# Optimization experiments

Measured on AMD Instinct MI355X. Metric: run time of the kernel, lower is better.

## Reference

```python
import jax, jax.numpy as jnp
import numpy as np

N = 50000      # nodes
E = 800000     # edges
INS = 128
H = 128
OUTS = 128
G = 512        # graphs in batch
BN_EPS = 1e-5


def _lin(k, fan_in, fan_out):
    s = 1.0 / np.sqrt(fan_in)
    kw, kb = jax.random.split(k)
    w = jax.random.uniform(kw, (fan_in, fan_out), minval=-s, maxval=s, dtype=jnp.float32)
    b = jax.random.uniform(kb, (fan_out,), minval=-s, maxval=s, dtype=jnp.float32)
    return w, b


def setup_inputs() -> dict:
    key = jax.random.key(0)
    ks = jax.random.split(key, 16)
    x = jax.random.normal(ks[0], (N, INS), dtype=jnp.float32)
    edge_src = jax.random.randint(ks[1], (E,), 0, N, dtype=jnp.int32)
    edge_dst = jax.random.randint(ks[2], (E,), 0, N, dtype=jnp.int32)
    ptr = jnp.sort(jax.random.randint(ks[3], (G + 1,), 0, N, dtype=jnp.int32))
    ptr = ptr.at[0].set(0).at[-1].set(N)
    w1a, b1a = _lin(ks[4], INS, H)
    w1b, b1b = _lin(ks[5], H, H)
    w2a, b2a = _lin(ks[6], H, H)
    w2b, b2b = _lin(ks[7], H, H)
    w3a, b3a = _lin(ks[8], H, H)
    w3b, b3b = _lin(ks[9], H, OUTS)
    g1 = jnp.ones((H,), jnp.float32); be1 = jnp.zeros((H,), jnp.float32)
    g2 = jnp.ones((H,), jnp.float32); be2 = jnp.zeros((H,), jnp.float32)
    g3 = jnp.ones((H,), jnp.float32); be3 = jnp.zeros((H,), jnp.float32)
    return dict(x=x, edge_src=edge_src, edge_dst=edge_dst, ptr=ptr,
                w1a=w1a, b1a=b1a, g1=g1, be1=be1, w1b=w1b, b1b=b1b,
                w2a=w2a, b2a=b2a, g2=g2, be2=be2, w2b=w2b, b2b=b2b,
                w3a=w3a, b3a=b3a, g3=g3, be3=be3, w3b=w3b, b3b=b3b)


def _bn(h, gamma, beta):
    # BatchNorm1d in training mode: stats over the node dimension
    mu = jnp.mean(h, axis=0)
    var = jnp.var(h, axis=0)
    return gamma * (h - mu) * jax.lax.rsqrt(var + BN_EPS) + beta


def _gin_layer(h, src, dst, wa, ba, gamma, beta, wb, bb):
    # GINConv (eps=0): mlp(x + sum_{j in N(i)} x_j)
    agg = jax.ops.segment_sum(h[src], dst, num_segments=N)  # [N, d]
    h = h + agg
    h = jax.nn.relu(_bn(h @ wa + ba, gamma, beta))
    h = jax.nn.relu(h @ wb + bb)
    return h


def reference(x, edge_src, edge_dst, ptr,
              w1a, b1a, g1, be1, w1b, b1b,
              w2a, b2a, g2, be2, w2b, b2b,
              w3a, b3a, g3, be3, w3b, b3b):
    h = _gin_layer(x, edge_src, edge_dst, w1a, b1a, g1, be1, w1b, b1b)
    h = _gin_layer(h, edge_src, edge_dst, w2a, b2a, g2, be2, w2b, b2b)
    h = _gin_layer(h, edge_src, edge_dst, w3a, b3a, g3, be3, w3b, b3b)
    # segment_csr(x, ptr, reduce='sum') readout
    seg = jnp.searchsorted(ptr, jnp.arange(N, dtype=jnp.int32), side='right') - 1
    return jax.ops.segment_sum(h, seg, num_segments=G)  # [G, OUTS]
```

## Files before the change

### kernel.cpp

```cpp
#include <hip/hip_runtime.h>

#define NNODES 50000
#define NEDGES 800000
#define HD 128
#define NG 512
#define BN_EPS 1e-5f
#define NTILE 3125
#define NSPLIT 8
#define NSB 49
#define AROW 136

typedef short bf16x8 __attribute__((ext_vector_type(8)));
typedef float floatx4 __attribute__((ext_vector_type(4)));

union U16 { uint4 u; bf16x8 h; };

__device__ __forceinline__ ushort f2bf(float f) {
    unsigned u = __float_as_uint(f);
    return (ushort)((u + 0x7fffu + ((u >> 16) & 1u)) >> 16);
}
__device__ __forceinline__ void unpack8(const uint4& u, float* f) {
    const unsigned* w = (const unsigned*)&u;
#pragma unroll
    for (int i = 0; i < 4; ++i) {
        f[2 * i]     = __uint_as_float(w[i] << 16);
        f[2 * i + 1] = __uint_as_float(w[i] & 0xffff0000u);
    }
}
__device__ __forceinline__ uint4 pack8(const float* f) {
    uint4 o;
    unsigned* w = (unsigned*)&o;
#pragma unroll
    for (int i = 0; i < 4; ++i)
        w[i] = (unsigned)f2bf(f[2 * i]) | ((unsigned)f2bf(f[2 * i + 1]) << 16);
    return o;
}


struct WP6 { const float* w[6]; };

__global__ __launch_bounds__(256) void prep_kernel(
    const int* __restrict__ edst, int* __restrict__ cnt,
    const float* __restrict__ x, ushort* __restrict__ xb,
    WP6 p, ushort* __restrict__ wf) {
    const int b = blockIdx.x, t = threadIdx.x;
    if (b < 3125) {
        atomicAdd(&cnt[edst[b * 256 + t]], 1);
    } else if (b < 9375) {
        int i = (b - 3125) * 256 + t;
        float4 v = ((const float4*)x)[i];
        ushort4 o;
        o.x = f2bf(v.x); o.y = f2bf(v.y); o.z = f2bf(v.z); o.w = f2bf(v.w);
        ((ushort4*)xb)[i] = o;
    } else {
        int m = b - 9375;
        const float* W = p.w[m];
        ushort* o = wf + (size_t)m * 16384;
        for (int i = t; i < 16384; i += 256) {
            int j = i & 7, lane = (i >> 3) & 63, kc = (i >> 9) & 3, ct = i >> 11;
            int k = kc * 32 + (lane >> 4) * 8 + j;
            int n = ct * 16 + (lane & 15);
            o[i] = f2bf(W[k * HD + n]);
        }
    }
}


__global__ void scan1_kernel(const int* __restrict__ cnt, int* __restrict__ incl,
                             int* __restrict__ bsum, int n) {
    __shared__ int s[1024];
    int i = blockIdx.x * 1024 + threadIdx.x;
    int v = (i < n) ? cnt[i] : 0;
    s[threadIdx.x] = v;
    __syncthreads();
    for (int off = 1; off < 1024; off <<= 1) {
        int add = (threadIdx.x >= off) ? s[threadIdx.x - off] : 0;
        __syncthreads();
        s[threadIdx.x] += add;
        __syncthreads();
    }
    if (i < n) incl[i] = s[threadIdx.x];
    if (threadIdx.x == 1023) bsum[blockIdx.x] = s[1023];
}

__global__ void scan23_kernel(const int* __restrict__ incl, const int* __restrict__ bsum,
                              int* __restrict__ rowp, int n) {
    __shared__ int bpre[64];
    const int t = threadIdx.x;
    if (t < 64) {
        int own = (t < NSB) ? bsum[t] : 0;
        int v = own;
        for (int off = 1; off < 64; off <<= 1) {
            int u = __shfl_up(v, off);
            if (t >= off) v += u;
        }
        bpre[t] = v - own;
    }
    __syncthreads();
    int i = blockIdx.x * 256 + t;
    if (i < n) rowp[i + 1] = incl[i] + bpre[i >> 10];
    if (i == 0) rowp[0] = 0;
}

__global__ void build_kernel(const int* __restrict__ src, const int* __restrict__ dst,
                             const int* __restrict__ rowp, int* __restrict__ fill,
                             int* __restrict__ colv, int n) {
    int i = blockIdx.x * 256 + threadIdx.x;
    if (i < n) {
        int d = dst[i];
        int pos = rowp[d] + atomicAdd(&fill[d], 1);
        colv[pos] = src[i];
    }
}


__global__ __launch_bounds__(256, 4) void gemmA_kernel(
    const ushort* __restrict__ H, const int* __restrict__ rowp,
    const int* __restrict__ colv, const ushort* __restrict__ Wf,
    const float* __restrict__ bias, ushort* __restrict__ out,
    float* __restrict__ ssum_p, float* __restrict__ ssq_p) {
    __shared__ ushort abuf[16 * AROW];
    __shared__ ushort cbuf[16 * HD];
    __shared__ float reds[HD];
    __shared__ float redq[HD];
    const int t = threadIdx.x;
    const int wave = t >> 6, lane = t & 63;
    const int quad = lane >> 4, l16 = lane & 15;
    const int row0 = blockIdx.x * 16;

    const uint4* Wf4 = (const uint4*)Wf;
    uint4 bfr[2][4];
#pragma unroll
    for (int c = 0; c < 2; ++c)
#pragma unroll
        for (int kc = 0; kc < 4; ++kc)
            bfr[c][kc] = Wf4[((2 * wave + c) * 4 + kc) * 64 + lane];

    {
        int nl = t >> 4;
        int node = row0 + nl;
        int l = t & 15;
        int beg = rowp[node], end = rowp[node + 1];
        const uint4* hp = (const uint4*)H;
        float a[8];
        unpack8(hp[(size_t)node * 16 + l], a);
        for (int j = beg; j < end; ++j) {
            float b[8];
            unpack8(hp[(size_t)colv[j] * 16 + l], b);
#pragma unroll
            for (int i = 0; i < 8; ++i) a[i] += b[i];
        }
        *(uint4*)&abuf[nl * AROW + l * 8] = pack8(a);
    }
    __syncthreads();

    U16 afr[4];
#pragma unroll
    for (int kc = 0; kc < 4; ++kc)
        afr[kc].u = *(const uint4*)&abuf[l16 * AROW + kc * 32 + quad * 8];

    floatx4 zf = {0.f, 0.f, 0.f, 0.f};
    floatx4 acc[2] = {zf, zf};
#pragma unroll
    for (int kc = 0; kc < 4; ++kc) {
#pragma unroll
        for (int c = 0; c < 2; ++c) {
            U16 bu;
            bu.u = bfr[c][kc];
            acc[c] = __builtin_amdgcn_mfma_f32_16x16x32_bf16(afr[kc].h, bu.h, acc[c], 0, 0, 0);
        }
    }

    const int lrow = quad * 4;
#pragma unroll
    for (int c = 0; c < 2; ++c) {
        int col = (2 * wave + c) * 16 + l16;
        float b = bias[col];
        float s = 0.f, q = 0.f;
#pragma unroll
        for (int reg = 0; reg < 4; ++reg) {
            float v = acc[c][reg] + b;
            cbuf[(lrow + reg) * HD + col] = f2bf(v);
            s += v; q += v * v;
        }
        s += __shfl_xor(s, 16); s += __shfl_xor(s, 32);
        q += __shfl_xor(q, 16); q += __shfl_xor(q, 32);
        if (quad == 0) { reds[col] = s; redq[col] = q; }
    }
    __syncthreads();

    {
        const uint4* c4 = (const uint4*)cbuf;
        uint4* o4 = (uint4*)out;
        int row = t >> 4, part = t & 15;
        o4[(size_t)(row0 + row) * 16 + part] = c4[t];
    }

    int slot = (blockIdx.x & (NSPLIT - 1)) * HD;
    if (t < HD) atomicAdd(&ssum_p[slot + t], reds[t]);
    else        atomicAdd(&ssq_p[slot + (t - HD)], redq[t - HD]);
}


template <bool READOUT>
__global__ __launch_bounds__(256, 4) void gemmB_kernel(
    const ushort* __restrict__ A, const ushort* __restrict__ Wf,
    const float* __restrict__ bias, ushort* __restrict__ out,
    const float* __restrict__ gamma, const float* __restrict__ beta,
    const float* __restrict__ ssum_p, const float* __restrict__ ssq_p,
    const int* __restrict__ gptr, float* __restrict__ gout) {
    __shared__ ushort cbuf[16 * HD];
    __shared__ float sca[HD];
    __shared__ float shf[HD];
    const int t = threadIdx.x;
    const int wave = t >> 6, lane = t & 63;
    const int quad = lane >> 4, l16 = lane & 15;
    const int row0 = blockIdx.x * 16;
    const int rowA = row0 + l16;

    const uint4* Wf4 = (const uint4*)Wf;
    uint4 bfr[2][4];
#pragma unroll
    for (int c = 0; c < 2; ++c)
#pragma unroll
        for (int kc = 0; kc < 4; ++kc)
            bfr[c][kc] = Wf4[((2 * wave + c) * 4 + kc) * 64 + lane];

    U16 afr[4];
    {
        const ushort* ap = A + (size_t)rowA * HD + quad * 8;
#pragma unroll
        for (int kc = 0; kc < 4; ++kc)
            afr[kc].u = *(const uint4*)(ap + kc * 32);
    }

    if (t < HD) {
        float s = 0.f, q = 0.f;
#pragma unroll
        for (int i = 0; i < NSPLIT; ++i) { s += ssum_p[i * HD + t]; q += ssq_p[i * HD + t]; }
        float mean = s / (float)NNODES;
        float var = q / (float)NNODES - mean * mean;
        float rstd = rsqrtf(var + BN_EPS);
        float sc = gamma[t] * rstd;
        sca[t] = sc;
        shf[t] = beta[t] - mean * sc;
    }
    __syncthreads();

#pragma unroll
    for (int kc = 0; kc < 4; ++kc) {
        float f[8];
        unpack8(afr[kc].u, f);
        int kb = kc * 32 + quad * 8;
        float4 s0 = ((const float4*)(sca + kb))[0];
        float4 s1 = ((const float4*)(sca + kb))[1];
        float4 h0 = ((const float4*)(shf + kb))[0];
        float4 h1 = ((const float4*)(shf + kb))[1];
        f[0] = fmaxf(fmaf(f[0], s0.x, h0.x), 0.f);
        f[1] = fmaxf(fmaf(f[1], s0.y, h0.y), 0.f);
        f[2] = fmaxf(fmaf(f[2], s0.z, h0.z), 0.f);
        f[3] = fmaxf(fmaf(f[3], s0.w, h0.w), 0.f);
        f[4] = fmaxf(fmaf(f[4], s1.x, h1.x), 0.f);
        f[5] = fmaxf(fmaf(f[5], s1.y, h1.y), 0.f);
        f[6] = fmaxf(fmaf(f[6], s1.z, h1.z), 0.f);
        f[7] = fmaxf(fmaf(f[7], s1.w, h1.w), 0.f);
        afr[kc].u = pack8(f);
    }

    floatx4 zf = {0.f, 0.f, 0.f, 0.f};
    floatx4 acc[2] = {zf, zf};
#pragma unroll
    for (int kc = 0; kc < 4; ++kc) {
#pragma unroll
        for (int c = 0; c < 2; ++c) {
            U16 bu;
            bu.u = bfr[c][kc];
            acc[c] = __builtin_amdgcn_mfma_f32_16x16x32_bf16(afr[kc].h, bu.h, acc[c], 0, 0, 0);
        }
    }

    if (READOUT) {
        int r_base = row0 + quad * 4;
        int lo = 0, hi = NG - 1;
        while (lo < hi) {
            int mid = (lo + hi) >> 1;
            if (r_base >= gptr[mid + 1]) lo = mid + 1; else hi = mid;
        }
        int segr[4];
        int sg = lo;
#pragma unroll
        for (int reg = 0; reg < 4; ++reg) {
            while (r_base + reg >= gptr[sg + 1]) ++sg;
            segr[reg] = sg;
        }
#pragma unroll
        for (int c = 0; c < 2; ++c) {
            int col = (2 * wave + c) * 16 + l16;
            float b = bias[col];
            float run = 0.f;
            int cur = segr[0];
#pragma unroll
            for (int reg = 0; reg < 4; ++reg) {
                if (segr[reg] != cur) {
                    if (run != 0.f) atomicAdd(&gout[cur * HD + col], run);
                    run = 0.f;
                    cur = segr[reg];
                }
                run += fmaxf(acc[c][reg] + b, 0.f);
            }
            if (run != 0.f) atomicAdd(&gout[cur * HD + col], run);
        }
        return;
    }

    const int lrow = quad * 4;
#pragma unroll
    for (int c = 0; c < 2; ++c) {
        int col = (2 * wave + c) * 16 + l16;
        float b = bias[col];
#pragma unroll
        for (int reg = 0; reg < 4; ++reg)
            cbuf[(lrow + reg) * HD + col] = f2bf(fmaxf(acc[c][reg] + b, 0.f));
    }
    __syncthreads();
    {
        const uint4* c4 = (const uint4*)cbuf;
        uint4* o4 = (uint4*)out;
        int row = t >> 4, part = t & 15;
        o4[(size_t)(row0 + row) * 16 + part] = c4[t];
    }
}


extern "C" void kernel_launch(void* const* d_in, const int* in_sizes, int n_in,
                              void* d_out, int out_size, void* d_ws, size_t ws_size,
                              hipStream_t stream) {
    const float* x = (const float*)d_in[0];
    const int* esrc = (const int*)d_in[1];
    const int* edst = (const int*)d_in[2];
    const int* gptr = (const int*)d_in[3];
    const float* wA[3] = {(const float*)d_in[4], (const float*)d_in[10], (const float*)d_in[16]};
    const float* bA[3] = {(const float*)d_in[5], (const float*)d_in[11], (const float*)d_in[17]};
    const float* gm[3] = {(const float*)d_in[6], (const float*)d_in[12], (const float*)d_in[18]};
    const float* bt[3] = {(const float*)d_in[7], (const float*)d_in[13], (const float*)d_in[19]};
    const float* wB[3] = {(const float*)d_in[8], (const float*)d_in[14], (const float*)d_in[20]};
    const float* bB[3] = {(const float*)d_in[9], (const float*)d_in[15], (const float*)d_in[21]};

    char* w = (char*)d_ws;
    ushort* xb   = (ushort*)w; w += (size_t)NNODES * HD * 2;
    ushort* zbb  = (ushort*)w; w += (size_t)NNODES * HD * 2;
    ushort* hbb  = (ushort*)w; w += (size_t)NNODES * HD * 2;
    ushort* wf   = (ushort*)w; w += (size_t)6 * 16384 * 2;
    int* colv  = (int*)w;   w += (size_t)NEDGES * 4;
    int* incl  = (int*)w;   w += (size_t)NNODES * 4;
    int* rowp  = (int*)w;   w += ((size_t)(NNODES + 1) * 4 + 15) & ~(size_t)15;
    int* bsum  = (int*)w;   w += 64 * 4;
    char* zero_base = w;
    int* cnt   = (int*)w;   w += (size_t)NNODES * 4;
    int* fill  = (int*)w;   w += (size_t)NNODES * 4;
    float* ssum_p = (float*)w; w += 3 * NSPLIT * 128 * 4;
    float* ssq_p  = (float*)w; w += 3 * NSPLIT * 128 * 4;
    size_t zero_bytes = (size_t)(w - zero_base);

    hipMemsetAsync(zero_base, 0, zero_bytes, stream);
    hipMemsetAsync(d_out, 0, (size_t)NG * HD * 4, stream);

    WP6 wp;
    wp.w[0] = wA[0]; wp.w[1] = wB[0]; wp.w[2] = wA[1];
    wp.w[3] = wB[1]; wp.w[4] = wA[2]; wp.w[5] = wB[2];

    prep_kernel<<<9381, 256, 0, stream>>>(edst, cnt, x, xb, wp, wf);
    scan1_kernel<<<NSB, 1024, 0, stream>>>(cnt, incl, bsum, NNODES);
    scan23_kernel<<<(NNODES + 255) / 256, 256, 0, stream>>>(incl, bsum, rowp, NNODES);
    build_kernel<<<(NEDGES + 255) / 256, 256, 0, stream>>>(esrc, edst, rowp, fill, colv, NEDGES);

    const ushort* hin = xb;
    for (int l = 0; l < 3; ++l) {
        gemmA_kernel<<<NTILE, 256, 0, stream>>>(
            hin, rowp, colv, wf + (size_t)(2 * l) * 16384, bA[l], zbb,
            ssum_p + l * NSPLIT * 128, ssq_p + l * NSPLIT * 128);
        if (l < 2) {
            gemmB_kernel<false><<<NTILE, 256, 0, stream>>>(
                zbb, wf + (size_t)(2 * l + 1) * 16384, bB[l], hbb, gm[l], bt[l],
                ssum_p + l * NSPLIT * 128, ssq_p + l * NSPLIT * 128, nullptr, nullptr);
        } else {
            gemmB_kernel<true><<<NTILE, 256, 0, stream>>>(
                zbb, wf + (size_t)(2 * l + 1) * 16384, bB[l], nullptr, gm[l], bt[l],
                ssum_p + l * NSPLIT * 128, ssq_p + l * NSPLIT * 128, gptr, (float*)d_out);
        }
        hin = hbb;
    }
}
```

Baseline: 422.0 us.

## Apply first linear before aggregation and fuse next layer's A-GEMM into B-GEMM

Uses linearity, (h+A h)W = hW + A(hW), so each layer's first GEMM runs before the neighbour gather. The gather kernel then sums projected rows, adds the bias and accumulates BN statistics, and each B-GEMM is fused with the following layer's A-GEMM, with that weight staged in LDS. The fp32-to-bf16 conversion of x moves into the first GEMM, and the CSR build reuses per-edge ranks from the counting atomics instead of a second atomic pass. The cost is an extra rank array, more LDS per block (lower occupancy), and rounding the projected features to bf16 before aggregation.

```diff
diff --git a/kernel.cpp b/kernel.cpp
--- a/kernel.cpp
+++ b/kernel.cpp
@@ -40,20 +40,14 @@
 struct WP6 { const float* w[6]; };
 
 __global__ __launch_bounds__(256) void prep_kernel(
-    const int* __restrict__ edst, int* __restrict__ cnt,
-    const float* __restrict__ x, ushort* __restrict__ xb,
+    const int* __restrict__ edst, int* __restrict__ cnt, int* __restrict__ rank,
     WP6 p, ushort* __restrict__ wf) {
     const int b = blockIdx.x, t = threadIdx.x;
     if (b < 3125) {
-        atomicAdd(&cnt[edst[b * 256 + t]], 1);
-    } else if (b < 9375) {
-        int i = (b - 3125) * 256 + t;
-        float4 v = ((const float4*)x)[i];
-        ushort4 o;
-        o.x = f2bf(v.x); o.y = f2bf(v.y); o.z = f2bf(v.z); o.w = f2bf(v.w);
-        ((ushort4*)xb)[i] = o;
+        int i = b * 256 + t;
+        rank[i] = atomicAdd(&cnt[edst[i]], 1);
     } else {
-        int m = b - 9375;
+        int m = b - 3125;
         const float* W = p.w[m];
         ushort* o = wf + (size_t)m * 16384;
         for (int i = t; i < 16384; i += 256) {
@@ -103,26 +97,18 @@
 }
 
 __global__ void build_kernel(const int* __restrict__ src, const int* __restrict__ dst,
-                             const int* __restrict__ rowp, int* __restrict__ fill,
+                             const int* __restrict__ rowp, const int* __restrict__ rank,
                              int* __restrict__ colv, int n) {
     int i = blockIdx.x * 256 + threadIdx.x;
-    if (i < n) {
-        int d = dst[i];
-        int pos = rowp[d] + atomicAdd(&fill[d], 1);
-        colv[pos] = src[i];
-    }
-}
-
-
-__global__ __launch_bounds__(256, 4) void gemmA_kernel(
-    const ushort* __restrict__ H, const int* __restrict__ rowp,
-    const int* __restrict__ colv, const ushort* __restrict__ Wf,
-    const float* __restrict__ bias, ushort* __restrict__ out,
-    float* __restrict__ ssum_p, float* __restrict__ ssq_p) {
+    if (i < n) colv[rowp[dst[i]] + rank[i]] = src[i];
+}
+
+
+__global__ __launch_bounds__(256, 4) void gemm0A_kernel(
+    const float* __restrict__ x, const ushort* __restrict__ Wf,
+    ushort* __restrict__ y) {
     __shared__ ushort abuf[16 * AROW];
     __shared__ ushort cbuf[16 * HD];
-    __shared__ float reds[HD];
-    __shared__ float redq[HD];
     const int t = threadIdx.x;
     const int wave = t >> 6, lane = t & 63;
     const int quad = lane >> 4, l16 = lane & 15;
@@ -137,20 +123,12 @@
             bfr[c][kc] = Wf4[((2 * wave + c) * 4 + kc) * 64 + lane];
 
     {
-        int nl = t >> 4;
-        int node = row0 + nl;
-        int l = t & 15;
-        int beg = rowp[node], end = rowp[node + 1];
-        const uint4* hp = (const uint4*)H;
-        float a[8];
-        unpack8(hp[(size_t)node * 16 + l], a);
-        for (int j = beg; j < end; ++j) {
-            float b[8];
-            unpack8(hp[(size_t)colv[j] * 16 + l], b);
-#pragma unroll
-            for (int i = 0; i < 8; ++i) a[i] += b[i];
-        }
-        *(uint4*)&abuf[nl * AROW + l * 8] = pack8(a);
+        int r = t >> 4, l = t & 15;
+        const float* xp = x + (size_t)(row0 + r) * HD + l * 8;
+        float4 v0 = ((const float4*)xp)[0];
+        float4 v1 = ((const float4*)xp)[1];
+        float f[8] = {v0.x, v0.y, v0.z, v0.w, v1.x, v1.y, v1.z, v1.w};
+        *(uint4*)&abuf[r * AROW + l * 8] = pack8(f);
     }
     __syncthreads();
 
@@ -162,54 +140,94 @@
     floatx4 zf = {0.f, 0.f, 0.f, 0.f};
     floatx4 acc[2] = {zf, zf};
 #pragma unroll
-    for (int kc = 0; kc < 4; ++kc) {
+    for (int kc = 0; kc < 4; ++kc)
 #pragma unroll
         for (int c = 0; c < 2; ++c) {
-            U16 bu;
-            bu.u = bfr[c][kc];
+            U16 bu; bu.u = bfr[c][kc];
             acc[c] = __builtin_amdgcn_mfma_f32_16x16x32_bf16(afr[kc].h, bu.h, acc[c], 0, 0, 0);
         }
-    }
 
     const int lrow = quad * 4;
 #pragma unroll
     for (int c = 0; c < 2; ++c) {
         int col = (2 * wave + c) * 16 + l16;
-        float b = bias[col];
-        float s = 0.f, q = 0.f;
-#pragma unroll
-        for (int reg = 0; reg < 4; ++reg) {
-            float v = acc[c][reg] + b;
-            cbuf[(lrow + reg) * HD + col] = f2bf(v);
-            s += v; q += v * v;
-        }
-        s += __shfl_xor(s, 16); s += __shfl_xor(s, 32);
-        q += __shfl_xor(q, 16); q += __shfl_xor(q, 32);
-        if (quad == 0) { reds[col] = s; redq[col] = q; }
-    }
-    __syncthreads();
-
+#pragma unroll
+        for (int reg = 0; reg < 4; ++reg)
+            cbuf[(lrow + reg) * HD + col] = f2bf(acc[c][reg]);
+    }
+    __syncthreads();
     {
         const uint4* c4 = (const uint4*)cbuf;
-        uint4* o4 = (uint4*)out;
+        uint4* o4 = (uint4*)y;
         int row = t >> 4, part = t & 15;
         o4[(size_t)(row0 + row) * 16 + part] = c4[t];
     }
-
+}
+
+
+__global__ __launch_bounds__(256) void agg_kernel(
+    const ushort* __restrict__ y, const int* __restrict__ rowp,
+    const int* __restrict__ colv, const float* __restrict__ bias,
+    ushort* __restrict__ z, float* __restrict__ ssum_p, float* __restrict__ ssq_p) {
+    __shared__ float reds[4][HD];
+    __shared__ float redq[4][HD];
+    const int t = threadIdx.x;
+    const int wave = t >> 6, lane = t & 63;
+    const int node = blockIdx.x * 16 + (t >> 4);
+    const int l = t & 15;
+    const uint4* hp = (const uint4*)y;
+
+    float a[8];
+    unpack8(hp[(size_t)node * 16 + l], a);
+    int beg = rowp[node], end = rowp[node + 1];
+    for (int j = beg; j < end; ++j) {
+        float b[8];
+        unpack8(hp[(size_t)colv[j] * 16 + l], b);
+#pragma unroll
+        for (int i = 0; i < 8; ++i) a[i] += b[i];
+    }
+    {
+        float4 b0 = ((const float4*)(bias + l * 8))[0];
+        float4 b1 = ((const float4*)(bias + l * 8))[1];
+        a[0] += b0.x; a[1] += b0.y; a[2] += b0.z; a[3] += b0.w;
+        a[4] += b1.x; a[5] += b1.y; a[6] += b1.z; a[7] += b1.w;
+    }
+    ((uint4*)z)[(size_t)node * 16 + l] = pack8(a);
+
+    float s[8], q[8];
+#pragma unroll
+    for (int i = 0; i < 8; ++i) { s[i] = a[i]; q[i] = a[i] * a[i]; }
+#pragma unroll
+    for (int i = 0; i < 8; ++i) {
+        s[i] += __shfl_xor(s[i], 16); s[i] += __shfl_xor(s[i], 32);
+        q[i] += __shfl_xor(q[i], 16); q[i] += __shfl_xor(q[i], 32);
+    }
+    if (lane < 16) {
+#pragma unroll
+        for (int i = 0; i < 8; ++i) {
+            reds[wave][lane * 8 + i] = s[i];
+            redq[wave][lane * 8 + i] = q[i];
+        }
+    }
+    __syncthreads();
     int slot = (blockIdx.x & (NSPLIT - 1)) * HD;
-    if (t < HD) atomicAdd(&ssum_p[slot + t], reds[t]);
-    else        atomicAdd(&ssq_p[slot + (t - HD)], redq[t - HD]);
-}
-
-
-template <bool READOUT>
-__global__ __launch_bounds__(256, 4) void gemmB_kernel(
-    const ushort* __restrict__ A, const ushort* __restrict__ Wf,
-    const float* __restrict__ bias, ushort* __restrict__ out,
+    if (t < HD) {
+        atomicAdd(&ssum_p[slot + t], reds[0][t] + reds[1][t] + reds[2][t] + reds[3][t]);
+    } else if (t < 2 * HD) {
+        int c = t - HD;
+        atomicAdd(&ssq_p[slot + c], redq[0][c] + redq[1][c] + redq[2][c] + redq[3][c]);
+    }
+}
+
+
+__global__ __launch_bounds__(256, 3) void gemmBA_kernel(
+    const ushort* __restrict__ z, const ushort* __restrict__ WfB,
+    const ushort* __restrict__ WfA2, const float* __restrict__ biasB,
+    ushort* __restrict__ yout,
     const float* __restrict__ gamma, const float* __restrict__ beta,
-    const float* __restrict__ ssum_p, const float* __restrict__ ssq_p,
-    const int* __restrict__ gptr, float* __restrict__ gout) {
-    __shared__ ushort cbuf[16 * HD];
+    const float* __restrict__ ssum_p, const float* __restrict__ ssq_p) {
+    __shared__ ushort was[16384];
+    __shared__ ushort cbuf[16 * AROW];
     __shared__ float sca[HD];
     __shared__ float shf[HD];
     const int t = threadIdx.x;
@@ -218,7 +236,17 @@
     const int row0 = blockIdx.x * 16;
     const int rowA = row0 + l16;
 
-    const uint4* Wf4 = (const uint4*)Wf;
+    {
+        const uint4* g = (const uint4*)WfA2;
+        uint4 v[8];
+#pragma unroll
+        for (int i = 0; i < 8; ++i) v[i] = g[i * 256 + t];
+        uint4* s = (uint4*)was;
+#pragma unroll
+        for (int i = 0; i < 8; ++i) s[i * 256 + t] = v[i];
+    }
+
+    const uint4* Wf4 = (const uint4*)WfB;
     uint4 bfr[2][4];
 #pragma unroll
     for (int c = 0; c < 2; ++c)
@@ -228,7 +256,7 @@
 
     U16 afr[4];
     {
-        const ushort* ap = A + (size_t)rowA * HD + quad * 8;
+        const ushort* ap = z + (size_t)rowA * HD + quad * 8;
 #pragma unroll
         for (int kc = 0; kc < 4; ++kc)
             afr[kc].u = *(const uint4*)(ap + kc * 32);
@@ -270,64 +298,157 @@
     floatx4 zf = {0.f, 0.f, 0.f, 0.f};
     floatx4 acc[2] = {zf, zf};
 #pragma unroll
-    for (int kc = 0; kc < 4; ++kc) {
+    for (int kc = 0; kc < 4; ++kc)
 #pragma unroll
         for (int c = 0; c < 2; ++c) {
-            U16 bu;
-            bu.u = bfr[c][kc];
+            U16 bu; bu.u = bfr[c][kc];
             acc[c] = __builtin_amdgcn_mfma_f32_16x16x32_bf16(afr[kc].h, bu.h, acc[c], 0, 0, 0);
         }
-    }
-
-    if (READOUT) {
-        int r_base = row0 + quad * 4;
-        int lo = 0, hi = NG - 1;
-        while (lo < hi) {
-            int mid = (lo + hi) >> 1;
-            if (r_base >= gptr[mid + 1]) lo = mid + 1; else hi = mid;
-        }
-        int segr[4];
-        int sg = lo;
-#pragma unroll
-        for (int reg = 0; reg < 4; ++reg) {
-            while (r_base + reg >= gptr[sg + 1]) ++sg;
-            segr[reg] = sg;
-        }
-#pragma unroll
-        for (int c = 0; c < 2; ++c) {
-            int col = (2 * wave + c) * 16 + l16;
-            float b = bias[col];
-            float run = 0.f;
-            int cur = segr[0];
-#pragma unroll
-            for (int reg = 0; reg < 4; ++reg) {
-                if (segr[reg] != cur) {
-                    if (run != 0.f) atomicAdd(&gout[cur * HD + col], run);
-                    run = 0.f;
-                    cur = segr[reg];
-                }
-                run += fmaxf(acc[c][reg] + b, 0.f);
-            }
-            if (run != 0.f) atomicAdd(&gout[cur * HD + col], run);
-        }
-        return;
-    }
 
     const int lrow = quad * 4;
 #pragma unroll
     for (int c = 0; c < 2; ++c) {
         int col = (2 * wave + c) * 16 + l16;
-        float b = bias[col];
+        float b = biasB[col];
 #pragma unroll
         for (int reg = 0; reg < 4; ++reg)
-            cbuf[(lrow + reg) * HD + col] = f2bf(fmaxf(acc[c][reg] + b, 0.f));
-    }
-    __syncthreads();
-    {
-        const uint4* c4 = (const uint4*)cbuf;
-        uint4* o4 = (uint4*)out;
+            cbuf[(lrow + reg) * AROW + col] = f2bf(fmaxf(acc[c][reg] + b, 0.f));
+    }
+    __syncthreads();
+
+    U16 a2[4];
+#pragma unroll
+    for (int kc = 0; kc < 4; ++kc)
+        a2[kc].u = *(const uint4*)&cbuf[l16 * AROW + kc * 32 + quad * 8];
+    const uint4* W2 = (const uint4*)was;
+    floatx4 acc2[2] = {zf, zf};
+#pragma unroll
+    for (int kc = 0; kc < 4; ++kc)
+#pragma unroll
+        for (int c = 0; c < 2; ++c) {
+            U16 bu; bu.u = W2[((2 * wave + c) * 4 + kc) * 64 + lane];
+            acc2[c] = __builtin_amdgcn_mfma_f32_16x16x32_bf16(a2[kc].h, bu.h, acc2[c], 0, 0, 0);
+        }
+    __syncthreads();
+
+#pragma unroll
+    for (int c = 0; c < 2; ++c) {
+        int col = (2 * wave + c) * 16 + l16;
+#pragma unroll
+        for (int reg = 0; reg < 4; ++reg)
+            cbuf[(lrow + reg) * AROW + col] = f2bf(acc2[c][reg]);
+    }
+    __syncthreads();
+    {
+        uint4* o4 = (uint4*)yout;
         int row = t >> 4, part = t & 15;
-        o4[(size_t)(row0 + row) * 16 + part] = c4[t];
+        o4[(size_t)(row0 + row) * 16 + part] = *(const uint4*)&cbuf[row * AROW + part * 8];
+    }
+}
+
+
+__global__ __launch_bounds__(256, 4) void gemmB2_kernel(
+    const ushort* __restrict__ z, const ushort* __restrict__ WfB,
+    const float* __restrict__ biasB,
+    const float* __restrict__ gamma, const float* __restrict__ beta,
+    const float* __restrict__ ssum_p, const float* __restrict__ ssq_p,
+    const int* __restrict__ gptr, float* __restrict__ gout) {
+    __shared__ float sca[HD];
+    __shared__ float shf[HD];
+    const int t = threadIdx.x;
+    const int wave = t >> 6, lane = t & 63;
+    const int quad = lane >> 4, l16 = lane & 15;
+    const int row0 = blockIdx.x * 16;
+    const int rowA = row0 + l16;
+
+    const uint4* Wf4 = (const uint4*)WfB;
+    uint4 bfr[2][4];
+#pragma unroll
+    for (int c = 0; c < 2; ++c)
+#pragma unroll
+        for (int kc = 0; kc < 4; ++kc)
+            bfr[c][kc] = Wf4[((2 * wave + c) * 4 + kc) * 64 + lane];
+
+    U16 afr[4];
+    {
+        const ushort* ap = z + (size_t)rowA * HD + quad * 8;
+#pragma unroll
+        for (int kc = 0; kc < 4; ++kc)
+            afr[kc].u = *(const uint4*)(ap + kc * 32);
+    }
+
+    if (t < HD) {
+        float s = 0.f, q = 0.f;
+#pragma unroll
+        for (int i = 0; i < NSPLIT; ++i) { s += ssum_p[i * HD + t]; q += ssq_p[i * HD + t]; }
+        float mean = s / (float)NNODES;
+        float var = q / (float)NNODES - mean * mean;
+        float rstd = rsqrtf(var + BN_EPS);
+        float sc = gamma[t] * rstd;
+        sca[t] = sc;
+        shf[t] = beta[t] - mean * sc;
+    }
+    __syncthreads();
+
+#pragma unroll
+    for (int kc = 0; kc < 4; ++kc) {
+        float f[8];
+        unpack8(afr[kc].u, f);
+        int kb = kc * 32 + quad * 8;
+        float4 s0 = ((const float4*)(sca + kb))[0];
+        float4 s1 = ((const float4*)(sca + kb))[1];
+        float4 h0 = ((const float4*)(shf + kb))[0];
+        float4 h1 = ((const float4*)(shf + kb))[1];
+        f[0] = fmaxf(fmaf(f[0], s0.x, h0.x), 0.f);
+        f[1] = fmaxf(fmaf(f[1], s0.y, h0.y), 0.f);
+        f[2] = fmaxf(fmaf(f[2], s0.z, h0.z), 0.f);
+        f[3] = fmaxf(fmaf(f[3], s0.w, h0.w), 0.f);
+        f[4] = fmaxf(fmaf(f[4], s1.x, h1.x), 0.f);
+        f[5] = fmaxf(fmaf(f[5], s1.y, h1.y), 0.f);
+        f[6] = fmaxf(fmaf(f[6], s1.z, h1.z), 0.f);
+        f[7] = fmaxf(fmaf(f[7], s1.w, h1.w), 0.f);
+        afr[kc].u = pack8(f);
+    }
+
+    floatx4 zf = {0.f, 0.f, 0.f, 0.f};
+    floatx4 acc[2] = {zf, zf};
+#pragma unroll
+    for (int kc = 0; kc < 4; ++kc)
+#pragma unroll
+        for (int c = 0; c < 2; ++c) {
+            U16 bu; bu.u = bfr[c][kc];
+            acc[c] = __builtin_amdgcn_mfma_f32_16x16x32_bf16(afr[kc].h, bu.h, acc[c], 0, 0, 0);
+        }
+
+    int r_base = row0 + quad * 4;
+    int lo = 0, hi = NG - 1;
+    while (lo < hi) {
+        int mid = (lo + hi) >> 1;
+        if (r_base >= gptr[mid + 1]) lo = mid + 1; else hi = mid;
+    }
+    int segr[4];
+    int sg = lo;
+#pragma unroll
+    for (int reg = 0; reg < 4; ++reg) {
+        while (r_base + reg >= gptr[sg + 1]) ++sg;
+        segr[reg] = sg;
+    }
+#pragma unroll
+    for (int c = 0; c < 2; ++c) {
+        int col = (2 * wave + c) * 16 + l16;
+        float b = biasB[col];
+        float run = 0.f;
+        int cur = segr[0];
+#pragma unroll
+        for (int reg = 0; reg < 4; ++reg) {
+            if (segr[reg] != cur) {
+                if (run != 0.f) atomicAdd(&gout[cur * HD + col], run);
+                run = 0.f;
+                cur = segr[reg];
+            }
+            run += fmaxf(acc[c][reg] + b, 0.f);
+        }
+        if (run != 0.f) atomicAdd(&gout[cur * HD + col], run);
     }
 }
 
@@ -347,17 +468,16 @@
     const float* bB[3] = {(const float*)d_in[9], (const float*)d_in[15], (const float*)d_in[21]};
 
     char* w = (char*)d_ws;
-    ushort* xb   = (ushort*)w; w += (size_t)NNODES * HD * 2;
-    ushort* zbb  = (ushort*)w; w += (size_t)NNODES * HD * 2;
-    ushort* hbb  = (ushort*)w; w += (size_t)NNODES * HD * 2;
+    ushort* ybuf = (ushort*)w; w += (size_t)NNODES * HD * 2;
+    ushort* zbuf = (ushort*)w; w += (size_t)NNODES * HD * 2;
     ushort* wf   = (ushort*)w; w += (size_t)6 * 16384 * 2;
     int* colv  = (int*)w;   w += (size_t)NEDGES * 4;
+    int* rank  = (int*)w;   w += (size_t)NEDGES * 4;
     int* incl  = (int*)w;   w += (size_t)NNODES * 4;
     int* rowp  = (int*)w;   w += ((size_t)(NNODES + 1) * 4 + 15) & ~(size_t)15;
     int* bsum  = (int*)w;   w += 64 * 4;
     char* zero_base = w;
     int* cnt   = (int*)w;   w += (size_t)NNODES * 4;
-    int* fill  = (int*)w;   w += (size_t)NNODES * 4;
     float* ssum_p = (float*)w; w += 3 * NSPLIT * 128 * 4;
     float* ssq_p  = (float*)w; w += 3 * NSPLIT * 128 * 4;
     size_t zero_bytes = (size_t)(w - zero_base);
@@ -369,25 +489,27 @@
     wp.w[0] = wA[0]; wp.w[1] = wB[0]; wp.w[2] = wA[1];
     wp.w[3] = wB[1]; wp.w[4] = wA[2]; wp.w[5] = wB[2];
 
-    prep_kernel<<<9381, 256, 0, stream>>>(edst, cnt, x, xb, wp, wf);
+    prep_kernel<<<3131, 256, 0, stream>>>(edst, cnt, rank, wp, wf);
     scan1_kernel<<<NSB, 1024, 0, stream>>>(cnt, incl, bsum, NNODES);
     scan23_kernel<<<(NNODES + 255) / 256, 256, 0, stream>>>(incl, bsum, rowp, NNODES);
-    build_kernel<<<(NEDGES + 255) / 256, 256, 0, stream>>>(esrc, edst, rowp, fill, colv, NEDGES);
-
-    const ushort* hin = xb;
+    build_kernel<<<(NEDGES + 255) / 256, 256, 0, stream>>>(esrc, edst, rowp, rank, colv, NEDGES);
+
+    gemm0A_kernel<<<NTILE, 256, 0, stream>>>(x, wf, ybuf);
+
     for (int l = 0; l < 3; ++l) {
-        gemmA_kernel<<<NTILE, 256, 0, stream>>>(
-            hin, rowp, colv, wf + (size_t)(2 * l) * 16384, bA[l], zbb,
+        agg_kernel<<<NTILE, 256, 0, stream>>>(
+            ybuf, rowp, colv, bA[l], zbuf,
             ssum_p + l * NSPLIT * 128, ssq_p + l * NSPLIT * 128);
         if (l < 2) {
-            gemmB_kernel<false><<<NTILE, 256, 0, stream>>>(
-                zbb, wf + (size_t)(2 * l + 1) * 16384, bB[l], hbb, gm[l], bt[l],
-                ssum_p + l * NSPLIT * 128, ssq_p + l * NSPLIT * 128, nullptr, nullptr);
+            gemmBA_kernel<<<NTILE, 256, 0, stream>>>(
+                zbuf, wf + (size_t)(2 * l + 1) * 16384, wf + (size_t)(2 * l + 2) * 16384,
+                bB[l], ybuf, gm[l], bt[l],
+                ssum_p + l * NSPLIT * 128, ssq_p + l * NSPLIT * 128);
         } else {
-            gemmB_kernel<true><<<NTILE, 256, 0, stream>>>(
-                zbb, wf + (size_t)(2 * l + 1) * 16384, bB[l], nullptr, gm[l], bt[l],
-                ssum_p + l * NSPLIT * 128, ssq_p + l * NSPLIT * 128, gptr, (float*)d_out);
-        }
-        hin = hbb;
-    }
-}
+            gemmB2_kernel<<<NTILE, 256, 0, stream>>>(
+                zbuf, wf + (size_t)(2 * l + 1) * 16384, bB[l], gm[l], bt[l],
+                ssum_p + l * NSPLIT * 128, ssq_p + l * NSPLIT * 128,
+                gptr, (float*)d_out);
+        }
+    }
+}
```

Result: faster. 402.9 us (-4.5%).
